# Kernel tuning notes

Hardware: AMD Instinct MI355X
Metric: run time of the kernel (lower is better)

The kernel has to match this reference:

```python
import jax, jax.numpy as jnp
import numpy as np

EPS = 1e-5
K = 20

def lrelu(x):
    return jnp.where(x >= 0, x, 0.2 * x)

def bn(x, g, b, axes):
    # training-mode batchnorm (biased variance), channel-last
    m = jnp.mean(x, axis=axes, keepdims=True)
    v = jnp.var(x, axis=axes, keepdims=True)
    return (x - m) * jax.lax.rsqrt(v + EPS) * g + b

def knn(xt, k):
    # xt: (B, N, C) -> (B, N, k) indices of k nearest (negative sq-dist topk, self included)
    sq = jnp.sum(xt * xt, axis=-1)                      # (B, N)
    pd = 2.0 * jnp.einsum('bnc,bmc->bnm', xt, xt) - sq[:, :, None] - sq[:, None, :]
    return jax.lax.top_k(pd, k)[1]

def graph_feature(xt, idx):
    # xt: (B, N, C), idx: (B, N, k) -> (B, N, k, 2C) = [neighbor - center, center]
    B = xt.shape[0]
    nb = xt[jnp.arange(B)[:, None, None], idx]          # (B, N, k, C)
    c = xt[:, :, None, :]
    return jnp.concatenate([nb - c, jnp.broadcast_to(c, nb.shape)], axis=-1)

def edge_block(h, w, g, b):
    # conv2d 1x1 (no bias) + BN2d + LeakyReLU, channel-last layout (B, N, k, C)
    h = jnp.einsum('bnkc,oc->bnko', h, w)
    return lrelu(bn(h, g, b, (0, 1, 2)))

def pt_block(h, w, g, b):
    # conv1d 1x1 (no bias) + BN1d + LeakyReLU, layout (B, N, C)
    h = jnp.einsum('bnc,oc->bno', h, w)
    return lrelu(bn(h, g, b, (0, 1)))

def setup_inputs() -> dict:
    key = jax.random.key(0)
    ks = jax.random.split(key, 16)
    B, C, N = 8, 9, 2048
    x = jax.random.normal(ks[0], (B, C, N), dtype=jnp.float32)
    shapes = [(64, 18), (64, 64), (64, 128), (64, 64), (64, 128),
              (1024, 192), (512, 1216), (256, 512)]
    d = {'x': x}
    for i, (o, ci) in enumerate(shapes):
        w = jax.random.normal(ks[i + 1], (o, ci), dtype=jnp.float32) / np.sqrt(ci)
        d[f'w{i+1}'] = w
        d[f'g{i+1}'] = jnp.ones((o,), dtype=jnp.float32)
        d[f'b{i+1}'] = jnp.zeros((o,), dtype=jnp.float32)
    return d

def reference(x, w1, g1, b1, w2, g2, b2, w3, g3, b3, w4, g4, b4,
              w5, g5, b5, w6, g6, b6, w7, g7, b7, w8, g8, b8):
    B, C, N = x.shape
    xt = jnp.transpose(x, (0, 2, 1))                    # (B, N, 9)
    inputs = xt
    # EdgeConv 1: knn on last 3 channels (dim9=True)
    h = graph_feature(xt, knn(xt[..., 6:], K))          # (B, N, k, 18)
    h = edge_block(h, w1, g1, b1)
    h = edge_block(h, w2, g2, b2)
    x1 = jnp.max(h, axis=2)                             # (B, N, 64)
    # EdgeConv 2
    h = graph_feature(x1, knn(x1, K))                   # (B, N, k, 128)
    h = edge_block(h, w3, g3, b3)
    h = edge_block(h, w4, g4, b4)
    x2 = jnp.max(h, axis=2)
    # EdgeConv 3
    h = graph_feature(x2, knn(x2, K))
    h = edge_block(h, w5, g5, b5)
    x3 = jnp.max(h, axis=2)
    # global feature
    h = pt_block(jnp.concatenate([x1, x2, x3], axis=-1), w6, g6, b6)  # (B, N, 1024)
    gmax = jnp.max(h, axis=1, keepdims=True)            # (B, 1, 1024)
    h = jnp.concatenate([jnp.broadcast_to(gmax, (B, N, gmax.shape[-1])), x1, x2, x3], axis=-1)
    h = pt_block(h, w7, g7, b7)                         # (B, N, 512)
    pf = pt_block(h, w8, g8, b8)                        # (B, N, 256)
    return inputs, jnp.transpose(pf, (0, 2, 1))         # (B,N,9), (B,256,N)
```

## Files before the change

kernel.cpp:

```cpp
#include <hip/hip_runtime.h>
#include <hip/hip_bf16.h>

typedef __hip_bfloat16 bf16;

#define BB 8
#define NN 2048
#define CC 9
#define KK 20
#define NSLOT 32

static constexpr int OFF_X1   = 0;
static constexpr int OFF_X2   = 1048576;
static constexpr int OFF_X3   = 2097152;
static constexpr int OFF_SQN  = 3145728;
static constexpr int OFF_GMAX = 3162112;
static constexpr int OFF_PART = 3170304;
static constexpr int OFF_STATS= 3432448;
static constexpr int OFF_IDX  = 3445248;
static constexpr int BASE_END = 3772928;

typedef __attribute__((ext_vector_type(8))) short bf16x8;
typedef __attribute__((ext_vector_type(4))) float f32x4;

__device__ __forceinline__ float lrelu(float x){ return x >= 0.f ? x : 0.2f * x; }

__device__ __forceinline__ void store4(float* p, float a, float b, float c, float d){
    *(float4*)p = make_float4(a,b,c,d);
}
__device__ __forceinline__ void store4(bf16* p, float a, float b, float c, float d){
    union { bf16 h[4]; uint2 u; } pk;
    pk.h[0] = (bf16)a; pk.h[1] = (bf16)b; pk.h[2] = (bf16)c; pk.h[3] = (bf16)d;
    *(uint2*)p = pk.u;
}

__device__ __forceinline__ void split2b(float v, bf16 &h, bf16 &l){
    h = (bf16)v;
    l = (bf16)(v - (float)h);
}

__device__ __forceinline__ unsigned f2sort(float f){
    unsigned b = __float_as_uint(f);
    return b ^ (unsigned)(((int)b >> 31) | (int)0x80000000);
}

__device__ __forceinline__ void fallback_extract(unsigned (&u)[32], int lane, int* __restrict__ orow){
    for (int it = 0; it < KK; it++){
        unsigned bv = u[0]; int bj = 0;
        #pragma unroll
        for (int j = 1; j < 32; j++) if (u[j] > bv){ bv = u[j]; bj = j; }
        int bm = bj*64 + lane;
        #pragma unroll
        for (int off = 32; off >= 1; off >>= 1){
            unsigned ov = __shfl_xor(bv, off);
            int om = __shfl_xor(bm, off);
            if (ov > bv || (ov == bv && om < bm)){ bv = ov; bm = om; }
        }
        if (lane == 0) orow[it] = bm;
        if ((bm & 63) == lane) u[bm >> 6] = 0u;
    }
}

__device__ __forceinline__ void topk20(unsigned (&u)[32], int lane,
                                       unsigned* sval, unsigned* sidx, int* __restrict__ orow){
    unsigned mx = 0u;
    #pragma unroll
    for (int j = 0; j < 32; j++) mx = (u[j] > mx) ? u[j] : mx;
    unsigned v = ~mx;
    #pragma unroll
    for (int k = 2; k <= 64; k <<= 1){
        #pragma unroll
        for (int j = k >> 1; j > 0; j >>= 1){
            unsigned o = __shfl_xor(v, j);
            bool keepMin = ((lane & k) == 0) == ((lane & j) == 0);
            bool less = (o < v);
            v = (keepMin == less) ? o : v;
        }
    }
    unsigned t0 = ~__shfl(v, 19);
    unsigned mask = 0u;
    #pragma unroll
    for (int j = 0; j < 32; j++) if (u[j] >= t0) mask |= (1u << j);
    int cnt = __popc(mask);
    int incl = cnt;
    #pragma unroll
    for (int off = 1; off < 64; off <<= 1){
        int t = __shfl_up(incl, off);
        if (lane >= off) incl += t;
    }
    int total = __shfl(incl, 63);
    if (total <= 64){
        int slot = incl - cnt;
        unsigned mm = mask;
        while (mm){
            int j = __ffs(mm) - 1;
            mm &= mm - 1u;
            sval[slot] = u[j];
            sidx[slot] = (unsigned)(j*64 + lane);
            slot++;
        }
        __threadfence_block();
        unsigned long long c = ~0ULL;
        if (lane < total)
            c = (((unsigned long long)(~sval[lane])) << 32) | (unsigned long long)sidx[lane];
        #pragma unroll
        for (int k = 2; k <= 64; k <<= 1){
            #pragma unroll
            for (int j = k >> 1; j > 0; j >>= 1){
                unsigned long long o = __shfl_xor(c, j);
                bool keepMin = ((lane & k) == 0) == ((lane & j) == 0);
                bool less = (o < c);
                c = (keepMin == less) ? o : c;
            }
        }
        if (lane < KK) orow[lane] = (int)(c & 0xffffffffULL);
    } else {
        fallback_extract(u, lane, orow);
    }
}

__global__ void k_echo(const float* __restrict__ x, float* __restrict__ out0){
    int t = blockIdx.x * 256 + threadIdx.x;
    if (t >= BB*CC*NN) return;
    int b = t / (CC*NN); int r = t % (CC*NN); int c = r / NN; int n = r % NN;
    out0[(b*NN + n)*CC + c] = x[t];
}

__global__ __launch_bounds__(256) void k_knn3(const float* __restrict__ x, int* __restrict__ idx){
    __shared__ float crd[NN*3];
    __shared__ unsigned sval[4*64];
    __shared__ unsigned sidx[4*64];
    int b  = blockIdx.x / (NN/4);
    int rb = blockIdx.x % (NN/4);
    for (int c = 0; c < 3; c++)
        for (int p = threadIdx.x; p < NN; p += 256)
            crd[p*3 + c] = x[(b*CC + 6 + c)*NN + p];
    __syncthreads();
    int lane = threadIdx.x & 63;
    int wid  = threadIdx.x >> 6;
    int n = rb*4 + wid;
    float qx = crd[n*3], qy = crd[n*3+1], qz = crd[n*3+2];
    float sqn = qx*qx + qy*qy + qz*qz;
    unsigned u[32];
    #pragma unroll
    for (int j = 0; j < 32; j++){
        int m = j*64 + lane;
        float mx = crd[m*3], my = crd[m*3+1], mz = crd[m*3+2];
        float d = 2.f*(qx*mx + qy*my + qz*mz) - sqn - (mx*mx + my*my + mz*mz);
        u[j] = f2sort(d);
    }
    topk20(u, lane, sval + wid*64, sidx + wid*64, idx + (b*NN + n)*KK);
}

__global__ __launch_bounds__(256) void k_pq9(const float* __restrict__ x, const float* __restrict__ w,
                                             float* __restrict__ P, float* __restrict__ Q){
    __shared__ __align__(16) float Xs[64*16];
    __shared__ __align__(16) float Wp[12*68];
    __shared__ __align__(16) float Wq[12*68];
    int row0 = blockIdx.x * 64;
    int b  = row0 >> 11;
    int n0 = row0 & (NN-1);
    int tx = threadIdx.x & 15, ty = threadIdx.x >> 4;
    for (int i = threadIdx.x; i < 64*12; i += 256){
        int r = i & 63, c = i >> 6;
        Xs[r*16 + c] = (c < 9) ? x[(b*CC + c)*NN + n0 + r] : 0.f;
    }
    for (int i = threadIdx.x; i < 64*12; i += 256){
        int c = i % 12, o = i / 12;
        float a = 0.f, dd = 0.f;
        if (c < 9){
            a  = w[o*18 + c];
            dd = w[o*18 + 9 + c] - a;
        }
        Wp[c*68 + o] = a;
        Wq[c*68 + o] = dd;
    }
    __syncthreads();
    float ap[4][4] = {{0.f}}, aq[4][4] = {{0.f}};
    for (int c0 = 0; c0 < 12; c0 += 4){
        float wp4[16], wq4[16];
        #pragma unroll
        for (int q = 0; q < 4; q++){
            *(float4*)&wp4[q*4] = *(const float4*)&Wp[(c0 + q)*68 + tx*4];
            *(float4*)&wq4[q*4] = *(const float4*)&Wq[(c0 + q)*68 + tx*4];
        }
        #pragma unroll
        for (int ii = 0; ii < 4; ii++){
            float4 x4 = *(const float4*)&Xs[(ty*4 + ii)*16 + c0];
            #pragma unroll
            for (int jj = 0; jj < 4; jj++){
                ap[ii][jj] += x4.x*wp4[jj] + x4.y*wp4[4+jj] + x4.z*wp4[8+jj] + x4.w*wp4[12+jj];
                aq[ii][jj] += x4.x*wq4[jj] + x4.y*wq4[4+jj] + x4.z*wq4[8+jj] + x4.w*wq4[12+jj];
            }
        }
    }
    #pragma unroll
    for (int ii = 0; ii < 4; ii++){
        int row = row0 + ty*4 + ii;
        store4(&P[row*64 + tx*4], ap[ii][0], ap[ii][1], ap[ii][2], ap[ii][3]);
        store4(&Q[row*64 + tx*4], aq[ii][0], aq[ii][1], aq[ii][2], aq[ii][3]);
    }
}

__global__ __launch_bounds__(256) void k_pq64(const float* __restrict__ X, const float* __restrict__ w,
                                              float* __restrict__ P, float* __restrict__ Q){
    __shared__ __align__(16) float Xs[64*68];
    __shared__ __align__(16) float Wp[64*68];
    __shared__ __align__(16) float Wq[64*68];
    int row0 = blockIdx.x * 64;
    int tx = threadIdx.x & 15, ty = threadIdx.x >> 4;
    for (int i = threadIdx.x; i < 64*64; i += 256){
        int c = i & 63, r = i >> 6;
        Xs[r*68 + c] = X[(row0 + r)*64 + c];
    }
    for (int i = threadIdx.x; i < 64*64; i += 256){
        int c = i & 63, o = i >> 6;
        float a  = w[o*128 + c];
        Wp[c*68 + o] = a;
        Wq[c*68 + o] = w[o*128 + 64 + c] - a;
    }
    __syncthreads();
    float ap[4][4] = {{0.f}}, aq[4][4] = {{0.f}};
    for (int c0 = 0; c0 < 64; c0 += 4){
        float wp4[16], wq4[16];
        #pragma unroll
        for (int q = 0; q < 4; q++){
            *(float4*)&wp4[q*4] = *(const float4*)&Wp[(c0 + q)*68 + tx*4];
            *(float4*)&wq4[q*4] = *(const float4*)&Wq[(c0 + q)*68 + tx*4];
        }
        #pragma unroll
        for (int ii = 0; ii < 4; ii++){
            float4 x4 = *(const float4*)&Xs[(ty*4 + ii)*68 + c0];
            #pragma unroll
            for (int jj = 0; jj < 4; jj++){
                ap[ii][jj] += x4.x*wp4[jj] + x4.y*wp4[4+jj] + x4.z*wp4[8+jj] + x4.w*wp4[12+jj];
                aq[ii][jj] += x4.x*wq4[jj] + x4.y*wq4[4+jj] + x4.z*wq4[8+jj] + x4.w*wq4[12+jj];
            }
        }
    }
    #pragma unroll
    for (int ii = 0; ii < 4; ii++){
        int row = row0 + ty*4 + ii;
        store4(&P[row*64 + tx*4], ap[ii][0], ap[ii][1], ap[ii][2], ap[ii][3]);
        store4(&Q[row*64 + tx*4], aq[ii][0], aq[ii][1], aq[ii][2], aq[ii][3]);
    }
}

template<bool DOMAX>
__global__ __launch_bounds__(256) void k_hstats(const float* __restrict__ P, const float* __restrict__ Q,
                                                const int* __restrict__ nbr, float* __restrict__ Xraw,
                                                double* __restrict__ dsum, double* __restrict__ dssq){
    __shared__ float sbuf[16*64];
    __shared__ float qbuf[16*64];
    int row0 = blockIdx.x * 80;
    int slot = blockIdx.x & (NSLOT-1);
    int tx = threadIdx.x & 15, ty = threadIdx.x >> 4;
    int ng = (row0 + ty*5) / 20;
    int b  = ng >> 11;
    float4 q4 = *(const float4*)&Q[ng*64 + tx*4];
    float s[4] = {0.f,0.f,0.f,0.f}, s2[4] = {0.f,0.f,0.f,0.f};
    float m[4] = {-INFINITY,-INFINITY,-INFINITY,-INFINITY};
    #pragma unroll
    for (int ii = 0; ii < 5; ii++){
        int e = row0 + ty*5 + ii;
        int j = nbr[e];
        float4 p4 = *(const float4*)&P[((b << 11) + j)*64 + tx*4];
        float h0 = p4.x + q4.x, h1 = p4.y + q4.y, h2 = p4.z + q4.z, h3 = p4.w + q4.w;
        s[0] += h0; s[1] += h1; s[2] += h2; s[3] += h3;
        s2[0] += h0*h0; s2[1] += h1*h1; s2[2] += h2*h2; s2[3] += h3*h3;
        if (DOMAX){
            m[0] = fmaxf(m[0], h0); m[1] = fmaxf(m[1], h1);
            m[2] = fmaxf(m[2], h2); m[3] = fmaxf(m[3], h3);
        }
    }
    #pragma unroll
    for (int jj = 0; jj < 4; jj++){
        sbuf[ty*64 + tx*4 + jj] = s[jj];
        qbuf[ty*64 + tx*4 + jj] = s2[jj];
    }
    if (DOMAX){
        #pragma unroll
        for (int off = 32; off >= 16; off >>= 1){
            #pragma unroll
            for (int jj = 0; jj < 4; jj++) m[jj] = fmaxf(m[jj], __shfl_xor(m[jj], off));
        }
        int lane = threadIdx.x & 63;
        if (lane < 16){
            int pi = ty >> 2;
            store4(&Xraw[(row0/20 + pi)*64 + tx*4], m[0], m[1], m[2], m[3]);
        }
    }
    __syncthreads();
    if (threadIdx.x < 64){
        double t = 0.0;
        #pragma unroll
        for (int k = 0; k < 16; k++) t += (double)sbuf[k*64 + threadIdx.x];
        atomicAdd(&dsum[slot*64 + threadIdx.x], t);
    } else if (threadIdx.x < 128){
        int c = threadIdx.x - 64;
        double t = 0.0;
        #pragma unroll
        for (int k = 0; k < 16; k++) t += (double)qbuf[k*64 + c];
        atomicAdd(&dssq[slot*64 + c], t);
    }
}

__global__ __launch_bounds__(256) void k_edgegemm(const float* __restrict__ P, const float* __restrict__ Q,
                                                  const int* __restrict__ nbr,
                                                  const float* __restrict__ sc, const float* __restrict__ sh,
                                                  const float* __restrict__ w,
                                                  float* __restrict__ Xraw,
                                                  double* __restrict__ dsum, double* __restrict__ dssq){
    __shared__ __align__(16) float Fs[80*68];
    __shared__ __align__(16) float Ws[64*68];
    int row0 = blockIdx.x * 80;
    int slot = blockIdx.x & (NSLOT-1);
    int tx = threadIdx.x & 15, ty = threadIdx.x >> 4;
    {
        int c4 = threadIdx.x & 15;
        float4 scv = *(const float4*)&sc[c4*4];
        float4 shv = *(const float4*)&sh[c4*4];
        for (int i = threadIdx.x; i < 80*16; i += 256){
            int r  = i >> 4;
            int e  = row0 + r;
            int ng = e / 20;
            int b  = ng >> 11;
            int j  = nbr[e];
            float4 p4 = *(const float4*)&P[((b << 11) + j)*64 + c4*4];
            float4 q4 = *(const float4*)&Q[ng*64 + c4*4];
            float4 f4;
            f4.x = lrelu((p4.x + q4.x)*scv.x + shv.x);
            f4.y = lrelu((p4.y + q4.y)*scv.y + shv.y);
            f4.z = lrelu((p4.z + q4.z)*scv.z + shv.z);
            f4.w = lrelu((p4.w + q4.w)*scv.w + shv.w);
            *(float4*)&Fs[r*68 + c4*4] = f4;
        }
    }
    for (int i = threadIdx.x; i < 64*16; i += 256){
        int o = i >> 4, c4 = i & 15;
        float4 w4 = *(const float4*)&w[o*64 + c4*4];
        Ws[(c4*4+0)*68 + o] = w4.x;
        Ws[(c4*4+1)*68 + o] = w4.y;
        Ws[(c4*4+2)*68 + o] = w4.z;
        Ws[(c4*4+3)*68 + o] = w4.w;
    }
    __syncthreads();
    float acc[5][4] = {{0.f}};
    for (int c0 = 0; c0 < 64; c0 += 4){
        float bb4[16];
        #pragma unroll
        for (int q = 0; q < 4; q++)
            *(float4*)&bb4[q*4] = *(const float4*)&Ws[(c0 + q)*68 + tx*4];
        #pragma unroll
        for (int ii = 0; ii < 5; ii++){
            float4 a4 = *(const float4*)&Fs[(ty*5 + ii)*68 + c0];
            #pragma unroll
            for (int jj = 0; jj < 4; jj++)
                acc[ii][jj] += a4.x*bb4[jj] + a4.y*bb4[4+jj] + a4.z*bb4[8+jj] + a4.w*bb4[12+jj];
        }
    }
    float s[4], q2[4], m[4];
    #pragma unroll
    for (int jj = 0; jj < 4; jj++){
        s[jj]  = acc[0][jj] + acc[1][jj] + acc[2][jj] + acc[3][jj] + acc[4][jj];
        q2[jj] = acc[0][jj]*acc[0][jj] + acc[1][jj]*acc[1][jj] + acc[2][jj]*acc[2][jj]
               + acc[3][jj]*acc[3][jj] + acc[4][jj]*acc[4][jj];
        m[jj]  = fmaxf(fmaxf(fmaxf(acc[0][jj], acc[1][jj]), fmaxf(acc[2][jj], acc[3][jj])), acc[4][jj]);
    }
    __syncthreads();
    float* sbuf = Fs;
    float* qbuf = Fs + 1024;
    #pragma unroll
    for (int jj = 0; jj < 4; jj++){
        sbuf[ty*64 + tx*4 + jj] = s[jj];
        qbuf[ty*64 + tx*4 + jj] = q2[jj];
    }
    #pragma unroll
    for (int off = 32; off >= 16; off >>= 1){
        #pragma unroll
        for (int jj = 0; jj < 4; jj++) m[jj] = fmaxf(m[jj], __shfl_xor(m[jj], off));
    }
    int lane = threadIdx.x & 63;
    if (lane < 16){
        int pi = ty >> 2;
        store4(&Xraw[(row0/20 + pi)*64 + tx*4], m[0], m[1], m[2], m[3]);
    }
    __syncthreads();
    if (threadIdx.x < 64){
        double t = 0.0;
        #pragma unroll
        for (int k = 0; k < 16; k++) t += (double)sbuf[k*64 + threadIdx.x];
        atomicAdd(&dsum[slot*64 + threadIdx.x], t);
    } else if (threadIdx.x < 128){
        int c = threadIdx.x - 64;
        double t = 0.0;
        #pragma unroll
        for (int k = 0; k < 16; k++) t += (double)qbuf[k*64 + c];
        atomicAdd(&dssq[slot*64 + c], t);
    }
}

__global__ void k_finalize(const double* __restrict__ dsum, const double* __restrict__ dssq,
                           const float* __restrict__ g, const float* __restrict__ b,
                           float* __restrict__ scale, float* __restrict__ shift,
                           int ch, double inv_cnt, int nslot){
    int c = blockIdx.x*256 + threadIdx.x;
    if (c >= ch) return;
    double sm = 0.0, sq = 0.0;
    for (int s = 0; s < nslot; s++){
        sm += dsum[s*ch + c];
        sq += dssq[s*ch + c];
    }
    double m = sm * inv_cnt;
    double v = sq * inv_cnt - m*m;
    if (v < 0.0) v = 0.0;
    float rs = (float)(1.0 / sqrt(v + 1e-5));
    float sc = g[c] * rs;
    scale[c] = sc;
    shift[c] = b[c] - (float)m*sc;
}

__global__ void k_bnact(float* __restrict__ X, const float* __restrict__ sc, const float* __restrict__ sh){
    int t = blockIdx.x*256 + threadIdx.x;
    int c = t & 63;
    X[t] = lrelu(X[t]*sc[c] + sh[c]);
}

__global__ void k_bnact8(float* __restrict__ O, const float* __restrict__ sc, const float* __restrict__ sh){
    int t = blockIdx.x*256 + threadIdx.x;
    int oc = (t >> 11) & 255;
    O[t] = lrelu(O[t]*sc[oc] + sh[oc]);
}

__global__ void k_sqnorm(const float* __restrict__ X, float* __restrict__ sqn){
    int row  = blockIdx.x*4 + (threadIdx.x >> 6);
    int lane = threadIdx.x & 63;
    float v = X[row*64 + lane];
    float s = v*v;
    #pragma unroll
    for (int off = 32; off >= 1; off >>= 1) s += __shfl_xor(s, off);
    if (lane == 0) sqn[row] = s;
}

__global__ __launch_bounds__(256) void k_gram2(const float* __restrict__ X, float* G0, float* G1, int b0){
    __shared__ __align__(16) float As[32*132];
    __shared__ __align__(16) float Bs[32*132];
    int sub = blockIdx.x >> 8;
    int t   = blockIdx.x & 255;
    const float* Xb = X + (size_t)(b0 + sub)*NN*64;
    float* gram = sub ? G1 : G0;
    int tr = t >> 4, tc = t & 15;
    int tx = threadIdx.x & 15, ty = threadIdx.x >> 4;
    float acc[8][8];
    #pragma unroll
    for (int i = 0; i < 8; i++)
        #pragma unroll
        for (int j = 0; j < 8; j++) acc[i][j] = 0.f;
    for (int kc0 = 0; kc0 < 64; kc0 += 32){
        __syncthreads();
        for (int i = threadIdx.x; i < 128*32; i += 256){
            int k = i & 31, r = i >> 5;
            As[k*132 + r] = Xb[(tr*128 + r)*64 + kc0 + k];
            Bs[k*132 + r] = Xb[(tc*128 + r)*64 + kc0 + k];
        }
        __syncthreads();
        for (int k = 0; k < 32; k++){
            float4 a0 = *(const float4*)&As[k*132 + ty*8];
            float4 a1 = *(const float4*)&As[k*132 + ty*8 + 4];
            float4 b0v = *(const float4*)&Bs[k*132 + tx*8];
            float4 b1v = *(const float4*)&Bs[k*132 + tx*8 + 4];
            float av[8] = {a0.x,a0.y,a0.z,a0.w,a1.x,a1.y,a1.z,a1.w};
            float bv[8] = {b0v.x,b0v.y,b0v.z,b0v.w,b1v.x,b1v.y,b1v.z,b1v.w};
            #pragma unroll
            for (int i = 0; i < 8; i++)
                #pragma unroll
                for (int j = 0; j < 8; j++) acc[i][j] += av[i]*bv[j];
        }
    }
    #pragma unroll
    for (int i = 0; i < 8; i++){
        int row = tr*128 + ty*8 + i;
        *(float4*)&gram[row*NN + tc*128 + tx*8]     = make_float4(acc[i][0],acc[i][1],acc[i][2],acc[i][3]);
        *(float4*)&gram[row*NN + tc*128 + tx*8 + 4] = make_float4(acc[i][4],acc[i][5],acc[i][6],acc[i][7]);
    }
}

__global__ __launch_bounds__(256) void k_sel2(const float* G0, const float* G1,
                                              const float* __restrict__ sqn, int* __restrict__ idx){
    __shared__ unsigned sval[4*64];
    __shared__ unsigned sidx[4*64];
    int sub = blockIdx.x >> 9;
    int rb  = blockIdx.x & 511;
    const float* gram = sub ? G1 : G0;
    const float* sq   = sqn + sub*NN;
    int lane = threadIdx.x & 63;
    int wid  = threadIdx.x >> 6;
    int n = rb*4 + wid;
    const float* grow = gram + (size_t)n*NN;
    float sn = sq[n];
    unsigned u[32];
    #pragma unroll
    for (int j = 0; j < 32; j++){
        int m = j*64 + lane;
        u[j] = f2sort(2.f*grow[m] - sn - sq[m]);
    }
    topk20(u, lane, sval + wid*64, sidx + wid*64, idx + (sub*NN + n)*KK);
}

__global__ __launch_bounds__(256) void k_c7(const float* __restrict__ gmax, const float* __restrict__ w7,
                                            float* __restrict__ C7){
    __shared__ float red[4*8];
    int oc = blockIdx.x;
    int tid = threadIdx.x, lane = tid & 63, wid = tid >> 6;
    float a[8];
    #pragma unroll
    for (int b = 0; b < 8; b++) a[b] = 0.f;
    for (int k = tid; k < 1024; k += 256){
        float wv = w7[oc*1216 + k];
        #pragma unroll
        for (int b = 0; b < 8; b++) a[b] += gmax[b*1024 + k] * wv;
    }
    #pragma unroll
    for (int b = 0; b < 8; b++){
        #pragma unroll
        for (int off = 32; off >= 1; off >>= 1) a[b] += __shfl_xor(a[b], off);
        if (lane == 0) red[wid*8 + b] = a[b];
    }
    __syncthreads();
    if (tid < 8){
        float s = red[tid] + red[8 + tid] + red[16 + tid] + red[24 + tid];
        C7[tid*512 + oc] = s;
    }
}

template<int MODE, bool MAXN, int STMODE, typename TST, typename TH7>
__global__ __launch_bounds__(256) void k_head(
    const float* __restrict__ X1, const float* __restrict__ X2, const float* __restrict__ X3,
    const TH7*  __restrict__ H7, const float* __restrict__ C7,
    const float* __restrict__ sc_in, const float* __restrict__ sh_in,
    const float* __restrict__ w,
    TST* __restrict__ HST, float* __restrict__ out1t, float* __restrict__ part,
    double* __restrict__ dsum, double* __restrict__ dssq)
{
    constexpr int CIN  = (MODE == 4) ? 512 : 192;
    constexpr int WST  = (MODE == 2) ? 192 : (MODE == 3 ? 1216 : 512);
    constexpr int WOFF = (MODE == 3) ? 1024 : 0;
    constexpr int COUT = (MODE == 2) ? 1024 : (MODE == 3 ? 512 : 256);
    constexpr int BM   = (MODE == 4) ? 64 : 128;
    constexpr int BN   = (MODE == 2) ? 128 : 64;
    constexpr int LOG2NRT = (BM == 64) ? 8 : 7;
    constexpr int RT2  = BM/64;
    constexpr int C2   = BN/16;
    constexpr int RPW  = BM/4;
    __shared__ __align__(16) char smem[(BM+BN)*128];
    constexpr int AH = 0, AL = BM*64, BH = 2*BM*64, BL = 2*BM*64 + BN*64;
    int tid = threadIdx.x;
    int rt = blockIdx.x & ((1 << LOG2NRT) - 1);
    int ct = blockIdx.x >> LOG2NRT;
    int row0 = rt * BM;
    int col0 = ct * BN;
    int b = row0 >> 11;
    int wv = tid >> 6, l = tid & 63;
    int rl = l & 15, g = l >> 4;

    f32x4 acc[RT2][C2];
    #pragma unroll
    for (int i = 0; i < RT2; i++)
        #pragma unroll
        for (int j = 0; j < C2; j++) acc[i][j] = (f32x4){0.f,0.f,0.f,0.f};

    for (int s = 0; s < CIN/32; s++){
        int cg0 = s*32;
        __syncthreads();
        #pragma unroll
        for (int it = 0; it < BM/64; it++){
            int i = tid + it*256;
            int r = i >> 2, kg = i & 3;
            float v[8];
            if (MODE == 4){
                float4 s0 = *(const float4*)&sc_in[cg0 + kg*8];
                float4 s1 = *(const float4*)&sc_in[cg0 + kg*8 + 4];
                float4 h0 = *(const float4*)&sh_in[cg0 + kg*8];
                float4 h1 = *(const float4*)&sh_in[cg0 + kg*8 + 4];
                float ss[8] = {s0.x,s0.y,s0.z,s0.w,s1.x,s1.y,s1.z,s1.w};
                float hh[8] = {h0.x,h0.y,h0.z,h0.w,h1.x,h1.y,h1.z,h1.w};
                if constexpr (sizeof(TH7) == 2){
                    union { uint4 q; unsigned short us[8]; } raw;
                    raw.q = *(const uint4*)&H7[(size_t)(row0 + r)*512 + cg0 + kg*8];
                    #pragma unroll
                    for (int e = 0; e < 8; e++)
                        v[e] = lrelu(__uint_as_float((unsigned)raw.us[e] << 16)*ss[e] + hh[e]);
                } else {
                    float4 a0 = *(const float4*)&H7[(size_t)(row0 + r)*512 + cg0 + kg*8];
                    float4 a1 = *(const float4*)&H7[(size_t)(row0 + r)*512 + cg0 + kg*8 + 4];
                    float av[8] = {a0.x,a0.y,a0.z,a0.w,a1.x,a1.y,a1.z,a1.w};
                    #pragma unroll
                    for (int e = 0; e < 8; e++) v[e] = lrelu(av[e]*ss[e] + hh[e]);
                }
            } else {
                const float* S = (cg0 < 64) ? X1 : (cg0 < 128 ? X2 : X3);
                int co = cg0 & 63;
                float4 a0 = *(const float4*)&S[(row0 + r)*64 + co + kg*8];
                float4 a1 = *(const float4*)&S[(row0 + r)*64 + co + kg*8 + 4];
                v[0]=a0.x; v[1]=a0.y; v[2]=a0.z; v[3]=a0.w;
                v[4]=a1.x; v[5]=a1.y; v[6]=a1.z; v[7]=a1.w;
            }
            union { bf16 h[8]; uint4 u; } ph, pl;
            #pragma unroll
            for (int e = 0; e < 8; e++) split2b(v[e], ph.h[e], pl.h[e]);
            *(uint4*)(smem + AH + r*64 + kg*16) = ph.u;
            *(uint4*)(smem + AL + r*64 + kg*16) = pl.u;
        }
        #pragma unroll
        for (int it = 0; it < BN/64; it++){
            int i = tid + it*256;
            int n = i >> 2, kg = i & 3;
            float4 b0 = *(const float4*)&w[(size_t)(col0 + n)*WST + WOFF + cg0 + kg*8];
            float4 b1 = *(const float4*)&w[(size_t)(col0 + n)*WST + WOFF + cg0 + kg*8 + 4];
            float v[8] = {b0.x,b0.y,b0.z,b0.w,b1.x,b1.y,b1.z,b1.w};
            union { bf16 h[8]; uint4 u; } ph, pl;
            #pragma unroll
            for (int e = 0; e < 8; e++) split2b(v[e], ph.h[e], pl.h[e]);
            *(uint4*)(smem + BH + n*64 + kg*16) = ph.u;
            *(uint4*)(smem + BL + n*64 + kg*16) = pl.u;
        }
        __syncthreads();
        #pragma unroll
        for (int rt2 = 0; rt2 < RT2; rt2++){
            int ar = (wv*RPW + rt2*16 + rl)*64 + g*16;
            bf16x8 ah = *(const bf16x8*)(smem + AH + ar);
            bf16x8 al = *(const bf16x8*)(smem + AL + ar);
            #pragma unroll
            for (int c2 = 0; c2 < C2; c2++){
                int br = (c2*16 + rl)*64 + g*16;
                bf16x8 bh = *(const bf16x8*)(smem + BH + br);
                bf16x8 bl = *(const bf16x8*)(smem + BL + br);
                acc[rt2][c2] = __builtin_amdgcn_mfma_f32_16x16x32_bf16(al, bh, acc[rt2][c2], 0, 0, 0);
                acc[rt2][c2] = __builtin_amdgcn_mfma_f32_16x16x32_bf16(ah, bl, acc[rt2][c2], 0, 0, 0);
                acc[rt2][c2] = __builtin_amdgcn_mfma_f32_16x16x32_bf16(ah, bh, acc[rt2][c2], 0, 0, 0);
            }
        }
    }
    if (MODE == 3){
        #pragma unroll
        for (int c2 = 0; c2 < C2; c2++){
            float c7 = C7[b*512 + col0 + c2*16 + rl];
            #pragma unroll
            for (int rt2 = 0; rt2 < RT2; rt2++)
                #pragma unroll
                for (int rr = 0; rr < 4; rr++) acc[rt2][c2][rr] += c7;
        }
    }
    if (STMODE == 1){
        #pragma unroll
        for (int rt2 = 0; rt2 < RT2; rt2++)
            #pragma unroll
            for (int c2 = 0; c2 < C2; c2++){
                int colg = col0 + c2*16 + rl;
                int rowg = row0 + wv*RPW + rt2*16 + g*4;
                #pragma unroll
                for (int rr = 0; rr < 4; rr++)
                    HST[(size_t)(rowg + rr)*COUT + colg] = (TST)acc[rt2][c2][rr];
            }
    } else if (STMODE == 2){
        int nb = (row0 & (NN-1)) + wv*RPW + g*4;
        #pragma unroll
        for (int rt2 = 0; rt2 < RT2; rt2++)
            #pragma unroll
            for (int c2 = 0; c2 < C2; c2++){
                float* o = out1t + b*256*NN + (size_t)(col0 + c2*16 + rl)*NN + nb + rt2*16;
                *(float4*)o = make_float4(acc[rt2][c2][0], acc[rt2][c2][1], acc[rt2][c2][2], acc[rt2][c2][3]);
            }
    }
    __syncthreads();
    float* sbuf = (float*)smem;
    float* qbuf = (float*)smem + 16*BN;
    float* mbuf = (float*)smem + 32*BN;
    int gi = wv*4 + g;
    #pragma unroll
    for (int c2 = 0; c2 < C2; c2++){
        float sv = 0.f, qv = 0.f, mv = -INFINITY;
        #pragma unroll
        for (int rt2 = 0; rt2 < RT2; rt2++)
            #pragma unroll
            for (int rr = 0; rr < 4; rr++){
                float v = acc[rt2][c2][rr];
                sv += v;
                qv += v*v;
                if (MAXN) mv = fmaxf(mv, v);
            }
        sbuf[gi*BN + c2*16 + rl] = sv;
        qbuf[gi*BN + c2*16 + rl] = qv;
        if (MAXN) mbuf[gi*BN + c2*16 + rl] = mv;
    }
    __syncthreads();
    if (tid < BN){
        double t = 0.0;
        #pragma unroll
        for (int k = 0; k < 16; k++) t += (double)sbuf[k*BN + tid];
        atomicAdd(&dsum[col0 + tid], t);
        if (MAXN){
            float mm = -INFINITY;
            #pragma unroll
            for (int k = 0; k < 16; k++) mm = fmaxf(mm, mbuf[k*BN + tid]);
            part[rt*1024 + col0 + tid] = mm;
        }
    } else if (tid < 2*BN){
        int c = tid - BN;
        double t = 0.0;
        #pragma unroll
        for (int k = 0; k < 16; k++) t += (double)qbuf[k*BN + c];
        atomicAdd(&dssq[col0 + c], t);
    }
}

__global__ void k_gmax_fin(const float* __restrict__ part, const float* __restrict__ sc,
                           const float* __restrict__ sh, float* __restrict__ gmax){
    int t = blockIdx.x*256 + threadIdx.x;
    int b = t >> 10, c = t & 1023;
    float m = -INFINITY;
    #pragma unroll
    for (int k = 0; k < 16; k++) m = fmaxf(m, part[(b*16 + k)*1024 + c]);
    gmax[t] = lrelu(m*sc[c] + sh[c]);
}

__global__ __launch_bounds__(256) void k_final_b(const bf16* __restrict__ H8,
                                                 const float* __restrict__ scale,
                                                 const float* __restrict__ shift,
                                                 float* __restrict__ out1){
    __shared__ float tile[64*65];
    int bi = blockIdx.x;
    int b  = bi / 128;
    int r  = bi % 128;
    int nt = r >> 2, ot = r & 3;
    for (int i = threadIdx.x; i < 64*64; i += 256){
        int o = i & 63, nl = i >> 6;
        float v = (float)H8[((b*NN) + nt*64 + nl)*256 + ot*64 + o];
        int oc = ot*64 + o;
        tile[o*65 + nl] = lrelu(v*scale[oc] + shift[oc]);
    }
    __syncthreads();
    for (int i = threadIdx.x; i < 64*64; i += 256){
        int nl = i & 63, o = i >> 6;
        out1[b*256*NN + (ot*64 + o)*NN + nt*64 + nl] = tile[o*65 + nl];
    }
}

extern "C" void kernel_launch(void* const* d_in, const int* in_sizes, int n_in,
                              void* d_out, int out_size, void* d_ws, size_t ws_size,
                              hipStream_t stream){
    const float* x = (const float*)d_in[0];
    const float *w[8], *g[8], *bb[8];
    for (int i = 0; i < 8; i++){
        w[i]  = (const float*)d_in[1 + i*3];
        g[i]  = (const float*)d_in[2 + i*3];
        bb[i] = (const float*)d_in[3 + i*3];
    }
    float* ws  = (float*)d_ws;
    float* X1  = ws + OFF_X1;
    float* X2  = ws + OFF_X2;
    float* X3  = ws + OFF_X3;
    float* SQN = ws + OFF_SQN;
    float* GMAX= ws + OFF_GMAX;
    float* PART= ws + OFF_PART;
    float* C7  = ws + OFF_PART + 131072;
    double* SLOTS = (double*)(ws + OFF_PART + 135168);
    double* DS = (double*)(ws + OFF_STATS);
    float*  FS = ws + OFF_STATS + 8448;
    int*   IDX = (int*)(ws + OFF_IDX);

    float* out0 = (float*)d_out;
    float* out1 = out0 + BB*NN*CC;
    float* P    = out1;
    float* Q    = out1 + 1048576;
    float* GRAM0= out1;
    float* GRAM1= ws + BASE_END;
    bool dualGram = ws_size >= (size_t)(BASE_END + 4194304)*4;

    const int chs[8]   = {64,64,64,64,64,1024,512,256};
    const int base[8]  = {0,128,256,384,512,640,2688,3712};
    double *SUMp[8], *SSQp[8];
    float  *SCp[8],  *SHp[8];
    for (int L = 0; L < 8; L++){
        if (L < 5){
            SUMp[L] = SLOTS + L*2*64*NSLOT;
            SSQp[L] = SLOTS + L*2*64*NSLOT + 64*NSLOT;
        } else {
            SUMp[L] = DS + base[L];
            SSQp[L] = DS + base[L] + chs[L];
        }
        SCp[L]  = FS + base[L];
        SHp[L]  = FS + base[L] + chs[L];
    }
    const double invE = 1.0 / (double)(BB*NN*KK);
    const double invP = 1.0 / (double)(BB*NN);

    hipMemsetAsync(DS, 0, 4224*sizeof(double), stream);
    hipMemsetAsync(SLOTS, 0, 5*2*64*NSLOT*sizeof(double), stream);
    k_echo<<<576,256,0,stream>>>(x, out0);

    k_knn3<<<BB*NN/4,256,0,stream>>>(x, IDX);
    k_pq9<<<256,256,0,stream>>>(x, w[0], P, Q);
    k_hstats<false><<<4096,256,0,stream>>>(P, Q, IDX, nullptr, SUMp[0], SSQp[0]);
    k_finalize<<<1,256,0,stream>>>(SUMp[0],SSQp[0],g[0],bb[0],SCp[0],SHp[0],64,invE,NSLOT);
    k_edgegemm<<<4096,256,0,stream>>>(P, Q, IDX, SCp[0], SHp[0], w[1], X1, SUMp[1], SSQp[1]);
    k_finalize<<<1,256,0,stream>>>(SUMp[1],SSQp[1],g[1],bb[1],SCp[1],SHp[1],64,invE,NSLOT);
    k_bnact<<<4096,256,0,stream>>>(X1, SCp[1], SHp[1]);

    for (int stage = 0; stage < 2; stage++){
        float* Xs = (stage == 0) ? X1 : X2;
        k_sqnorm<<<4096,256,0,stream>>>(Xs, SQN);
        if (dualGram){
            for (int pr = 0; pr < 4; pr++){
                k_gram2<<<512,256,0,stream>>>(Xs, GRAM0, GRAM1, pr*2);
                k_sel2<<<1024,256,0,stream>>>(GRAM0, GRAM1, SQN + pr*2*NN, IDX + pr*2*NN*KK);
            }
        } else {
            for (int b = 0; b < BB; b++){
                k_gram2<<<256,256,0,stream>>>(Xs, GRAM0, GRAM0, b);
                k_sel2<<<512,256,0,stream>>>(GRAM0, GRAM0, SQN + b*NN, IDX + b*NN*KK);
            }
        }
        if (stage == 0){
            k_pq64<<<256,256,0,stream>>>(X1, w[2], P, Q);
            k_hstats<false><<<4096,256,0,stream>>>(P, Q, IDX, nullptr, SUMp[2], SSQp[2]);
            k_finalize<<<1,256,0,stream>>>(SUMp[2],SSQp[2],g[2],bb[2],SCp[2],SHp[2],64,invE,NSLOT);
            k_edgegemm<<<4096,256,0,stream>>>(P, Q, IDX, SCp[2], SHp[2], w[3], X2, SUMp[3], SSQp[3]);
            k_finalize<<<1,256,0,stream>>>(SUMp[3],SSQp[3],g[3],bb[3],SCp[3],SHp[3],64,invE,NSLOT);
            k_bnact<<<4096,256,0,stream>>>(X2, SCp[3], SHp[3]);
        } else {
            k_pq64<<<256,256,0,stream>>>(X2, w[4], P, Q);
            k_hstats<true><<<4096,256,0,stream>>>(P, Q, IDX, X3, SUMp[4], SSQp[4]);
            k_finalize<<<1,256,0,stream>>>(SUMp[4],SSQp[4],g[4],bb[4],SCp[4],SHp[4],64,invE,NSLOT);
            k_bnact<<<4096,256,0,stream>>>(X3, SCp[4], SHp[4]);
        }
    }

    k_head<2,true,0,float,float><<<1024,256,0,stream>>>(
        X1,X2,X3,(const float*)nullptr,nullptr,nullptr,nullptr,w[5],
        (float*)nullptr,nullptr,PART,SUMp[5],SSQp[5]);
    k_finalize<<<4,256,0,stream>>>(SUMp[5],SSQp[5],g[5],bb[5],SCp[5],SHp[5],1024,invP,1);
    k_gmax_fin<<<32,256,0,stream>>>(PART, SCp[5], SHp[5], GMAX);
    k_c7<<<512,256,0,stream>>>(GMAX, w[6], C7);

    if (ws_size >= (size_t)12161536*4){
        float* H7f = ws + BASE_END;
        k_head<3,false,1,float,float><<<1024,256,0,stream>>>(
            X1,X2,X3,(const float*)nullptr,C7,nullptr,nullptr,w[6],
            H7f,nullptr,nullptr,SUMp[6],SSQp[6]);
        k_finalize<<<2,256,0,stream>>>(SUMp[6],SSQp[6],g[6],bb[6],SCp[6],SHp[6],512,invP,1);
        k_head<4,false,2,float,float><<<1024,256,0,stream>>>(
            nullptr,nullptr,nullptr,H7f,nullptr,SCp[6],SHp[6],w[7],
            (float*)nullptr,out1,nullptr,SUMp[7],SSQp[7]);
        k_finalize<<<1,256,0,stream>>>(SUMp[7],SSQp[7],g[7],bb[7],SCp[7],SHp[7],256,invP,1);
        k_bnact8<<<16384,256,0,stream>>>(out1, SCp[7], SHp[7]);
    } else if (ws_size >= (size_t)7967232*4){
        bf16* H7b = (bf16*)(ws + BASE_END);
        k_head<3,false,1,bf16,float><<<1024,256,0,stream>>>(
            X1,X2,X3,(const float*)nullptr,C7,nullptr,nullptr,w[6],
            H7b,nullptr,nullptr,SUMp[6],SSQp[6]);
        k_finalize<<<2,256,0,stream>>>(SUMp[6],SSQp[6],g[6],bb[6],SCp[6],SHp[6],512,invP,1);
        k_head<4,false,2,float,bf16><<<1024,256,0,stream>>>(
            nullptr,nullptr,nullptr,H7b,nullptr,SCp[6],SHp[6],w[7],
            (float*)nullptr,out1,nullptr,SUMp[7],SSQp[7]);
        k_finalize<<<1,256,0,stream>>>(SUMp[7],SSQp[7],g[7],bb[7],SCp[7],SHp[7],256,invP,1);
        k_bnact8<<<16384,256,0,stream>>>(out1, SCp[7], SHp[7]);
    } else {
        bf16* H7b = (bf16*)out1;
        bf16* H8b = (bf16*)(ws + OFF_X1);
        k_head<3,false,1,bf16,float><<<1024,256,0,stream>>>(
            X1,X2,X3,(const float*)nullptr,C7,nullptr,nullptr,w[6],
            H7b,nullptr,nullptr,SUMp[6],SSQp[6]);
        k_finalize<<<2,256,0,stream>>>(SUMp[6],SSQp[6],g[6],bb[6],SCp[6],SHp[6],512,invP,1);
        k_head<4,false,1,bf16,bf16><<<1024,256,0,stream>>>(
            nullptr,nullptr,nullptr,H7b,nullptr,SCp[6],SHp[6],w[7],
            H8b,nullptr,nullptr,SUMp[7],SSQp[7]);
        k_finalize<<<1,256,0,stream>>>(SUMp[7],SSQp[7],g[7],bb[7],SCp[7],SHp[7],256,invP,1);
        k_final_b<<<1024,256,0,stream>>>(H8b, SCp[7], SHp[7], out1);
    }
}
```

Measured before the change: 745.5 us.

## Exploit Gram symmetry, vectorize BN activations, repad edge GEMM weight tile

```diff
diff --git a/kernel.cpp b/kernel.cpp
--- a/kernel.cpp
+++ b/kernel.cpp
@@ -311,7 +311,7 @@
                                                   float* __restrict__ Xraw,
                                                   double* __restrict__ dsum, double* __restrict__ dssq){
     __shared__ __align__(16) float Fs[80*68];
-    __shared__ __align__(16) float Ws[64*68];
+    __shared__ __align__(16) float Ws[64*65];
     int row0 = blockIdx.x * 80;
     int slot = blockIdx.x & (NSLOT-1);
     int tx = threadIdx.x & 15, ty = threadIdx.x >> 4;
@@ -335,13 +335,9 @@
             *(float4*)&Fs[r*68 + c4*4] = f4;
         }
     }
-    for (int i = threadIdx.x; i < 64*16; i += 256){
-        int o = i >> 4, c4 = i & 15;
-        float4 w4 = *(const float4*)&w[o*64 + c4*4];
-        Ws[(c4*4+0)*68 + o] = w4.x;
-        Ws[(c4*4+1)*68 + o] = w4.y;
-        Ws[(c4*4+2)*68 + o] = w4.z;
-        Ws[(c4*4+3)*68 + o] = w4.w;
+    for (int i = threadIdx.x; i < 64*64; i += 256){
+        int c = i & 63, o = i >> 6;
+        Ws[c*65 + o] = w[o*64 + c];
     }
     __syncthreads();
     float acc[5][4] = {{0.f}};
@@ -349,7 +345,7 @@
         float bb4[16];
         #pragma unroll
         for (int q = 0; q < 4; q++)
-            *(float4*)&bb4[q*4] = *(const float4*)&Ws[(c0 + q)*68 + tx*4];
+            *(float4*)&bb4[q*4] = *(const float4*)&Ws[(c0 + q)*65 + tx*4];
         #pragma unroll
         for (int ii = 0; ii < 5; ii++){
             float4 a4 = *(const float4*)&Fs[(ty*5 + ii)*68 + c0];
@@ -421,14 +417,27 @@
 
 __global__ void k_bnact(float* __restrict__ X, const float* __restrict__ sc, const float* __restrict__ sh){
     int t = blockIdx.x*256 + threadIdx.x;
-    int c = t & 63;
-    X[t] = lrelu(X[t]*sc[c] + sh[c]);
+    int e0 = t*4;
+    int c0 = e0 & 63;
+    float4 v = *(float4*)&X[e0];
+    v.x = lrelu(v.x*sc[c0+0] + sh[c0+0]);
+    v.y = lrelu(v.y*sc[c0+1] + sh[c0+1]);
+    v.z = lrelu(v.z*sc[c0+2] + sh[c0+2]);
+    v.w = lrelu(v.w*sc[c0+3] + sh[c0+3]);
+    *(float4*)&X[e0] = v;
 }
 
 __global__ void k_bnact8(float* __restrict__ O, const float* __restrict__ sc, const float* __restrict__ sh){
     int t = blockIdx.x*256 + threadIdx.x;
-    int oc = (t >> 11) & 255;
-    O[t] = lrelu(O[t]*sc[oc] + sh[oc]);
+    int e0 = t*4;
+    int oc = (e0 >> 11) & 255;
+    float s = sc[oc], h = sh[oc];
+    float4 v = *(float4*)&O[e0];
+    v.x = lrelu(v.x*s + h);
+    v.y = lrelu(v.y*s + h);
+    v.z = lrelu(v.z*s + h);
+    v.w = lrelu(v.w*s + h);
+    *(float4*)&O[e0] = v;
 }
 
 __global__ void k_sqnorm(const float* __restrict__ X, float* __restrict__ sqn){
@@ -444,11 +453,13 @@
 __global__ __launch_bounds__(256) void k_gram2(const float* __restrict__ X, float* G0, float* G1, int b0){
     __shared__ __align__(16) float As[32*132];
     __shared__ __align__(16) float Bs[32*132];
-    int sub = blockIdx.x >> 8;
-    int t   = blockIdx.x & 255;
+    int sub = blockIdx.x / 136;
+    int t   = blockIdx.x % 136;
+    int tr = 0;
+    while (t >= 16 - tr){ t -= 16 - tr; tr++; }
+    int tc = tr + t;
     const float* Xb = X + (size_t)(b0 + sub)*NN*64;
     float* gram = sub ? G1 : G0;
-    int tr = t >> 4, tc = t & 15;
     int tx = threadIdx.x & 15, ty = threadIdx.x >> 4;
     float acc[8][8];
     #pragma unroll
@@ -479,8 +490,16 @@
     #pragma unroll
     for (int i = 0; i < 8; i++){
         int row = tr*128 + ty*8 + i;
-        *(float4*)&gram[row*NN + tc*128 + tx*8]     = make_float4(acc[i][0],acc[i][1],acc[i][2],acc[i][3]);
-        *(float4*)&gram[row*NN + tc*128 + tx*8 + 4] = make_float4(acc[i][4],acc[i][5],acc[i][6],acc[i][7]);
+        *(float4*)&gram[(size_t)row*NN + tc*128 + tx*8]     = make_float4(acc[i][0],acc[i][1],acc[i][2],acc[i][3]);
+        *(float4*)&gram[(size_t)row*NN + tc*128 + tx*8 + 4] = make_float4(acc[i][4],acc[i][5],acc[i][6],acc[i][7]);
+    }
+    if (tr != tc){
+        #pragma unroll
+        for (int j = 0; j < 8; j++){
+            int col = tc*128 + tx*8 + j;
+            *(float4*)&gram[(size_t)col*NN + tr*128 + ty*8]     = make_float4(acc[0][j],acc[1][j],acc[2][j],acc[3][j]);
+            *(float4*)&gram[(size_t)col*NN + tr*128 + ty*8 + 4] = make_float4(acc[4][j],acc[5][j],acc[6][j],acc[7][j]);
+        }
     }
 }
 
@@ -804,19 +823,19 @@
     k_finalize<<<1,256,0,stream>>>(SUMp[0],SSQp[0],g[0],bb[0],SCp[0],SHp[0],64,invE,NSLOT);
     k_edgegemm<<<4096,256,0,stream>>>(P, Q, IDX, SCp[0], SHp[0], w[1], X1, SUMp[1], SSQp[1]);
     k_finalize<<<1,256,0,stream>>>(SUMp[1],SSQp[1],g[1],bb[1],SCp[1],SHp[1],64,invE,NSLOT);
-    k_bnact<<<4096,256,0,stream>>>(X1, SCp[1], SHp[1]);
+    k_bnact<<<1024,256,0,stream>>>(X1, SCp[1], SHp[1]);
 
     for (int stage = 0; stage < 2; stage++){
         float* Xs = (stage == 0) ? X1 : X2;
         k_sqnorm<<<4096,256,0,stream>>>(Xs, SQN);
         if (dualGram){
             for (int pr = 0; pr < 4; pr++){
-                k_gram2<<<512,256,0,stream>>>(Xs, GRAM0, GRAM1, pr*2);
+                k_gram2<<<272,256,0,stream>>>(Xs, GRAM0, GRAM1, pr*2);
                 k_sel2<<<1024,256,0,stream>>>(GRAM0, GRAM1, SQN + pr*2*NN, IDX + pr*2*NN*KK);
             }
         } else {
             for (int b = 0; b < BB; b++){
-                k_gram2<<<256,256,0,stream>>>(Xs, GRAM0, GRAM0, b);
+                k_gram2<<<136,256,0,stream>>>(Xs, GRAM0, GRAM0, b);
                 k_sel2<<<512,256,0,stream>>>(GRAM0, GRAM0, SQN + b*NN, IDX + b*NN*KK);
             }
         }
@@ -826,12 +845,12 @@
             k_finalize<<<1,256,0,stream>>>(SUMp[2],SSQp[2],g[2],bb[2],SCp[2],SHp[2],64,invE,NSLOT);
             k_edgegemm<<<4096,256,0,stream>>>(P, Q, IDX, SCp[2], SHp[2], w[3], X2, SUMp[3], SSQp[3]);
             k_finalize<<<1,256,0,stream>>>(SUMp[3],SSQp[3],g[3],bb[3],SCp[3],SHp[3],64,invE,NSLOT);
-            k_bnact<<<4096,256,0,stream>>>(X2, SCp[3], SHp[3]);
+            k_bnact<<<1024,256,0,stream>>>(X2, SCp[3], SHp[3]);
         } else {
             k_pq64<<<256,256,0,stream>>>(X2, w[4], P, Q);
             k_hstats<true><<<4096,256,0,stream>>>(P, Q, IDX, X3, SUMp[4], SSQp[4]);
             k_finalize<<<1,256,0,stream>>>(SUMp[4],SSQp[4],g[4],bb[4],SCp[4],SHp[4],64,invE,NSLOT);
-            k_bnact<<<4096,256,0,stream>>>(X3, SCp[4], SHp[4]);
+            k_bnact<<<1024,256,0,stream>>>(X3, SCp[4], SHp[4]);
         }
     }
 
@@ -852,7 +871,7 @@
             nullptr,nullptr,nullptr,H7f,nullptr,SCp[6],SHp[6],w[7],
             (float*)nullptr,out1,nullptr,SUMp[7],SSQp[7]);
         k_finalize<<<1,256,0,stream>>>(SUMp[7],SSQp[7],g[7],bb[7],SCp[7],SHp[7],256,invP,1);
-        k_bnact8<<<16384,256,0,stream>>>(out1, SCp[7], SHp[7]);
+        k_bnact8<<<4096,256,0,stream>>>(out1, SCp[7], SHp[7]);
     } else if (ws_size >= (size_t)7967232*4){
         bf16* H7b = (bf16*)(ws + BASE_END);
         k_head<3,false,1,bf16,float><<<1024,256,0,stream>>>(
@@ -863,7 +882,7 @@
             nullptr,nullptr,nullptr,H7b,nullptr,SCp[6],SHp[6],w[7],
             (float*)nullptr,out1,nullptr,SUMp[7],SSQp[7]);
         k_finalize<<<1,256,0,stream>>>(SUMp[7],SSQp[7],g[7],bb[7],SCp[7],SHp[7],256,invP,1);
-        k_bnact8<<<16384,256,0,stream>>>(out1, SCp[7], SHp[7]);
+        k_bnact8<<<4096,256,0,stream>>>(out1, SCp[7], SHp[7]);
     } else {
         bf16* H7b = (bf16*)out1;
         bf16* H8b = (bf16*)(ws + OFF_X1);
```

Measured after the change: 770.7 us. 3.4% more time.
